# Kernel optimization log

Measured on AMD Instinct MI355X. Metric: run time of the kernel, lower is better.

Reference implementation:

```python
import jax, jax.numpy as jnp
import numpy as np

B, L, N, D, H, R = 4, 4096, 1024, 768, 12, 8
HD = D // H
LORA_SCALE = 16.0 / 8.0
EPS = 1e-5

def _layernorm(x, g, b):
    mu = jnp.mean(x, axis=-1, keepdims=True)
    var = jnp.mean(jnp.square(x - mu), axis=-1, keepdims=True)
    return (x - mu) * jax.lax.rsqrt(var + EPS) * g + b

def setup_inputs() -> dict:
    key = jax.random.key(0)
    ks = jax.random.split(key, 16)
    s = 0.02
    return {
        "text": jax.random.normal(ks[0], (B, L, D), jnp.float32),
        "regions": jax.random.normal(ks[1], (B, N, D), jnp.float32),
        "region_mask": jax.random.randint(ks[2], (B, N), 0, 2) > 0,
        "Wq": jax.random.normal(ks[3], (D, D), jnp.float32) * s,
        "Aq": jax.random.normal(ks[4], (R, D), jnp.float32) * s,
        "Bq": jax.random.normal(ks[5], (D, R), jnp.float32) * s,
        "Wk": jax.random.normal(ks[6], (D, D), jnp.float32) * s,
        "Wv": jax.random.normal(ks[7], (D, D), jnp.float32) * s,
        "Av": jax.random.normal(ks[8], (R, D), jnp.float32) * s,
        "Bv": jax.random.normal(ks[9], (D, R), jnp.float32) * s,
        "Wo": jax.random.normal(ks[10], (D, D), jnp.float32) * s,
        "bo": jnp.zeros((D,), jnp.float32),
        "gq": jnp.ones((D,), jnp.float32),
        "bq_ln": jnp.zeros((D,), jnp.float32),
        "gkv": jnp.ones((D,), jnp.float32),
        "bkv": jnp.zeros((D,), jnp.float32),
    }

def reference(text, regions, region_mask, Wq, Aq, Bq, Wk, Wv, Av, Bv, Wo, bo, gq, bq_ln, gkv, bkv):
    # pre-norms
    tq = _layernorm(text, gq, bq_ln)          # (B,L,D)
    rk = _layernorm(regions, gkv, bkv)        # (B,N,D)
    # LoRA-adapted projections (weights stored as (out,in), torch convention)
    Q = tq @ Wq.T + LORA_SCALE * ((tq @ Aq.T) @ Bq.T)
    K = rk @ Wk.T
    V = regions @ Wv.T + LORA_SCALE * ((regions @ Av.T) @ Bv.T)
    Q = Q.reshape(B, L, H, HD)
    K = K.reshape(B, N, H, HD)
    V = V.reshape(B, N, H, HD)
    scale = HD ** -0.5
    attn = jnp.einsum('blhd,bnhd->bhln', Q, K) * scale   # (B,H,L,N)
    bad = ~region_mask[:, None, None, :]
    attn = jnp.where(bad, -jnp.inf, attn)
    attn = jax.nn.softmax(attn, axis=-1)
    attn = jnp.nan_to_num(attn, nan=0.0)                 # fully-masked rows -> 0
    # dropout: eval mode (identity)
    out = jnp.einsum('bhln,bnhd->blhd', attn, V).reshape(B, L, D)
    return text + out @ Wo.T + bo
```

## Files before the change

### kernel.cpp

```cpp
#include <hip/hip_runtime.h>
#include <cstdint>
#include <cstddef>

#define B_  4
#define L_  4096
#define N_  1024
#define D_  768
#define H_  12
#define HD_ 64

typedef __bf16 bf16x4 __attribute__((ext_vector_type(4)));
typedef __bf16 bf16x8 __attribute__((ext_vector_type(8)));
typedef float  f32x4  __attribute__((ext_vector_type(4)));
typedef unsigned int u32;

static __device__ __forceinline__ f32x4 mfma16(bf16x8 a, bf16x8 b, f32x4 c) {
    return __builtin_amdgcn_mfma_f32_16x16x32_bf16(a, b, c, 0, 0, 0);
}

static __device__ __forceinline__ void async_cp16(const __bf16* g, const __bf16* l) {
    __builtin_amdgcn_global_load_lds(
        (const __attribute__((address_space(1))) u32*)g,
        (__attribute__((address_space(3))) u32*)l, 16, 0, 0);
}

static __device__ __forceinline__ u32 pkbf(float lo, float hi) {
    union { __bf16 b[2]; u32 u; } r;
    r.b[0] = (__bf16)lo; r.b[1] = (__bf16)hi;
    return r.u;
}


static __device__ __forceinline__ void ln_row(const float* __restrict__ xr,
                                              const float* __restrict__ g,
                                              const float* __restrict__ be,
                                              __bf16* __restrict__ yr)
{
    const int tid = threadIdx.x, lane = tid & 63, wid = tid >> 6;
    float4 v = make_float4(0.f, 0.f, 0.f, 0.f);
    if (tid < 192) v = *(const float4*)(xr + tid * 4);
    float s  = v.x + v.y + v.z + v.w;
    float s2 = v.x * v.x + v.y * v.y + v.z * v.z + v.w * v.w;
#pragma unroll
    for (int off = 32; off > 0; off >>= 1) {
        s  += __shfl_down(s, off);
        s2 += __shfl_down(s2, off);
    }
    __shared__ float red[8];
    if (lane == 0) { red[wid] = s; red[4 + wid] = s2; }
    __syncthreads();
    s  = red[0] + red[1] + red[2] + red[3];
    s2 = red[4] + red[5] + red[6] + red[7];
    const float mean = s * (1.f / D_);
    const float var  = s2 * (1.f / D_) - mean * mean;
    const float rstd = rsqrtf(var + 1e-5f);
    if (tid < 192) {
        const float4 gv = *(const float4*)(g + tid * 4);
        const float4 bv = *(const float4*)(be + tid * 4);
        bf16x4 o;
        o[0] = (__bf16)((v.x - mean) * rstd * gv.x + bv.x);
        o[1] = (__bf16)((v.y - mean) * rstd * gv.y + bv.y);
        o[2] = (__bf16)((v.z - mean) * rstd * gv.z + bv.z);
        o[3] = (__bf16)((v.w - mean) * rstd * gv.w + bv.w);
        *(bf16x4*)(yr + tid * 4) = o;
    }
}

static __device__ __forceinline__ void cast4(const float* __restrict__ in,
                                             __bf16* __restrict__ out, int blk)
{
    const int i = (blk * 256 + threadIdx.x) * 4;
    const float4 v = *(const float4*)(in + i);
    bf16x4 o;
    o[0] = (__bf16)v.x; o[1] = (__bf16)v.y; o[2] = (__bf16)v.z; o[3] = (__bf16)v.w;
    *(bf16x4*)(out + i) = o;
}

static __device__ __forceinline__ void weff4(const float* __restrict__ W,
                                             const float* __restrict__ Bm,
                                             const float* __restrict__ Am,
                                             __bf16* __restrict__ out, int blk)
{
    const int idx = (blk * 256 + threadIdx.x) * 4;
    const int o = idx / D_, i = idx - o * D_;
    const float4 w = *(const float4*)(W + idx);
    float sx = 0.f, sy = 0.f, sz = 0.f, sw = 0.f;
#pragma unroll
    for (int r = 0; r < 8; ++r) {
        const float b = Bm[o * 8 + r];
        const float4 a = *(const float4*)(Am + r * D_ + i);
        sx += b * a.x; sy += b * a.y; sz += b * a.z; sw += b * a.w;
    }
    bf16x4 ov;
    ov[0] = (__bf16)(w.x + 2.f * sx);
    ov[1] = (__bf16)(w.y + 2.f * sy);
    ov[2] = (__bf16)(w.z + 2.f * sz);
    ov[3] = (__bf16)(w.w + 2.f * sw);
    *(bf16x4*)(out + idx) = ov;
}

static __device__ __forceinline__ void compact_mask(const int* __restrict__ mask,
                                                    int* __restrict__ idxm,
                                                    int* __restrict__ Nv)
{
    const int tid = threadIdx.x, lane = tid & 63, wid = tid >> 6;
    const int4 mv = *(const int4*)(mask + tid * 4);
    const int v0 = mv.x != 0, v1 = mv.y != 0, v2 = mv.z != 0, v3 = mv.w != 0;
    const int c = v0 + v1 + v2 + v3;
    int incl = c;
#pragma unroll
    for (int off = 1; off < 64; off <<= 1) {
        const int n = __shfl_up(incl, off);
        if (lane >= off) incl += n;
    }
    __shared__ int wsum[4];
    if (lane == 63) wsum[wid] = incl;
    __syncthreads();
    int base = 0;
    for (int w = 0; w < wid; ++w) base += wsum[w];
    int p = base + incl - c;
    idxm[tid * 4 + 0] = v0 ? p : -1; p += v0;
    idxm[tid * 4 + 1] = v1 ? p : -1; p += v1;
    idxm[tid * 4 + 2] = v2 ? p : -1; p += v2;
    idxm[tid * 4 + 3] = v3 ? p : -1; p += v3;
    if (tid == 255) *Nv = p;
}

__global__ __launch_bounds__(256) void prologue_kernel(
    const float* __restrict__ text, const float* __restrict__ regions,
    const int* __restrict__ mask,
    const float* __restrict__ Wq, const float* __restrict__ Aq, const float* __restrict__ Bq,
    const float* __restrict__ Wv, const float* __restrict__ Av, const float* __restrict__ Bv,
    const float* __restrict__ Wk, const float* __restrict__ Wo,
    const float* __restrict__ gq, const float* __restrict__ bq,
    const float* __restrict__ gkv, const float* __restrict__ bkv,
    __bf16* __restrict__ tq, __bf16* __restrict__ rk, __bf16* __restrict__ regb,
    __bf16* __restrict__ Weq, __bf16* __restrict__ Wev,
    __bf16* __restrict__ Wkb, __bf16* __restrict__ Wob,
    int* __restrict__ idx_map, int* __restrict__ NvArr)
{
    int bx = blockIdx.x;
    if (bx < B_ * L_) { ln_row(text + (size_t)bx * D_, gq, bq, tq + (size_t)bx * D_); return; }
    bx -= B_ * L_;
    if (bx < B_ * N_) { ln_row(regions + (size_t)bx * D_, gkv, bkv, rk + (size_t)bx * D_); return; }
    bx -= B_ * N_;
    if (bx < 3072) { cast4(regions, regb, bx); return; }
    bx -= 3072;
    if (bx < 576) { weff4(Wq, Bq, Aq, Weq, bx); return; }
    bx -= 576;
    if (bx < 576) { weff4(Wv, Bv, Av, Wev, bx); return; }
    bx -= 576;
    if (bx < 576) { cast4(Wk, Wkb, bx); return; }
    bx -= 576;
    if (bx < 576) { cast4(Wo, Wob, bx); return; }
    bx -= 576;
    compact_mask(mask + bx * N_, idx_map + bx * N_, NvArr + bx);
}

template <int EPI, typename CT>
static __device__ __forceinline__ void gemm_body(__bf16* sm,
                                                 const __bf16* __restrict__ A,
                                                 const __bf16* __restrict__ W,
                                                 CT* __restrict__ C,
                                                 const float* __restrict__ resid,
                                                 const float* __restrict__ bias,
                                                 const int* __restrict__ idxm,
                                                 int mb0, int nb0)
{
    const int tid = threadIdx.x, wid = tid >> 6, lane = tid & 63;
    const int lr = lane & 15, g = lane >> 4;
    const int wm = wid >> 1, wn = wid & 1;

    auto skey2 = [](int row) { return (row >> 1) & 3; };

    auto stage = [&](int kb, int buf) {
        __bf16* as = sm + buf * 8192;
        __bf16* bs = as + 4096;
#pragma unroll
        for (int j = 0; j < 2; ++j) {
            const int s = wid * 64 + lane + j * 256;
            const int row = s >> 2;
            const int c = (s & 3) ^ skey2(row);
            const int dst = (wid * 64 + j * 256) * 8;
            async_cp16(A + (size_t)(mb0 + row) * D_ + kb * 32 + c * 8, as + dst);
            async_cp16(W + (size_t)(nb0 + row) * D_ + kb * 32 + c * 8, bs + dst);
        }
    };

    f32x4 acc[4][4] = {};

    stage(0, 0);
    asm volatile("s_waitcnt vmcnt(0)" ::: "memory");
    __syncthreads();

    for (int kb = 0; kb < D_ / 32; ++kb) {
        const int buf = kb & 1;
        if (kb < D_ / 32 - 1) stage(kb + 1, buf ^ 1);
        const __bf16* as = sm + buf * 8192;
        const __bf16* bs = as + 4096;
        bf16x8 av[4], wv[4];
#pragma unroll
        for (int mi = 0; mi < 4; ++mi) {
            const int row = wm * 64 + mi * 16 + lr;
            av[mi] = *(const bf16x8*)(as + row * 32 + (g ^ skey2(row)) * 8);
        }
#pragma unroll
        for (int oi = 0; oi < 4; ++oi) {
            const int row = wn * 64 + oi * 16 + lr;
            wv[oi] = *(const bf16x8*)(bs + row * 32 + (g ^ skey2(row)) * 8);
        }
        __builtin_amdgcn_s_setprio(1);
#pragma unroll
        for (int mi = 0; mi < 4; ++mi)
#pragma unroll
            for (int oi = 0; oi < 4; ++oi)
                acc[mi][oi] = mfma16(av[mi], wv[oi], acc[mi][oi]);
        __builtin_amdgcn_s_setprio(0);
        asm volatile("s_waitcnt vmcnt(0)" ::: "memory");
        __syncthreads();
    }

#pragma unroll
    for (int mi = 0; mi < 4; ++mi) {
#pragma unroll
        for (int oi = 0; oi < 4; ++oi) {
#pragma unroll
            for (int r = 0; r < 4; ++r) {
                const int m = mb0 + wm * 64 + mi * 16 + g * 4 + r;
                const int o = nb0 + wn * 64 + oi * 16 + lr;
                float v = acc[mi][oi][r];
                if (EPI == 2)
                    v += resid[(size_t)m * D_ + o] + bias[o];
                if (EPI == 3)
                    v *= 0.125f;
                if (EPI == 4) {
                    const int pos = idxm[m];
                    if (pos >= 0)
                        C[((size_t)((m >> 10) << 10) + pos) * D_ + o] = (CT)v;
                } else if (EPI == 5) {
                    const int pos = idxm[m];
                    if (pos >= 0)
                        C[((size_t)((m >> 10) * H_ + (o >> 6)) * HD_ + (o & 63)) * N_ + pos] = (CT)v;
                } else {
                    C[(size_t)m * D_ + o] = (CT)v;
                }
            }
        }
    }
}

__global__ __launch_bounds__(256) void gemm_qkv(const __bf16* __restrict__ tq,
                                                const __bf16* __restrict__ Weq,
                                                __bf16* __restrict__ Qb,
                                                const __bf16* __restrict__ rk,
                                                const __bf16* __restrict__ Wkb,
                                                __bf16* __restrict__ Kb,
                                                const __bf16* __restrict__ regb,
                                                const __bf16* __restrict__ Wev,
                                                __bf16* __restrict__ Vt,
                                                const int* __restrict__ idx_map)
{
    extern __shared__ __bf16 smem[];
    const int bx = blockIdx.x, ny = blockIdx.y * 128;
    if (bx < 128)      gemm_body<3, __bf16>(smem, tq,   Weq, Qb, nullptr, nullptr, nullptr, bx * 128, ny);
    else if (bx < 160) gemm_body<4, __bf16>(smem, rk,   Wkb, Kb, nullptr, nullptr, idx_map, (bx - 128) * 128, ny);
    else               gemm_body<5, __bf16>(smem, regb, Wev, Vt, nullptr, nullptr, idx_map, (bx - 160) * 128, ny);
}

__global__ __launch_bounds__(256) void gemm_out(const __bf16* __restrict__ A,
                                                const __bf16* __restrict__ W,
                                                float* __restrict__ C,
                                                const float* __restrict__ resid,
                                                const float* __restrict__ bias)
{
    extern __shared__ __bf16 smem[];
    gemm_body<2, float>(smem, A, W, C, resid, bias, nullptr, blockIdx.x * 128, blockIdx.y * 128);
}

__global__ __launch_bounds__(256, 3) void attn_kernel(const __bf16* __restrict__ Qb,
                                                      const __bf16* __restrict__ Kb,
                                                      const __bf16* __restrict__ Vt,
                                                      const int* __restrict__ NvArr,
                                                      __bf16* __restrict__ ctx)
{
    const int bq = blockIdx.x, h = blockIdx.y, b = blockIdx.z;
    const int tid = threadIdx.x, wid = tid >> 6, lane = tid & 63;
    const int lr = lane & 15, g = lane >> 4;

    const int Nv = NvArr[b];
    const int ntiles = (Nv + 63) >> 6;

    __shared__ float maskadd[N_];
    __shared__ __align__(16) __bf16 kbuf[2][4096];
    __shared__ __align__(16) __bf16 vbuf[2][4096];

    for (int i = tid; i < N_; i += 256)
        maskadd[i] = (i < Nv) ? 0.f : -1e30f;

    const int hoff = h * HD_;
    const int bN = b * N_;
    const size_t bhHD = ((size_t)b * H_ + h) * HD_;

    auto skey = [](int row) { return (row & 3) | (((row >> 3) & 1) << 2); };

    auto stage = [&](int t, int bsel) {
        const int n0 = t * 64;
#pragma unroll
        for (int j = 0; j < 2; ++j) {
            const int s = wid * 64 + lane + j * 256;
            const int row = s >> 3;
            const int ks = (s & 7) ^ skey(row);
            const int dst = (wid * 64 + j * 256) * 8;
            async_cp16(Kb + ((size_t)(bN + n0 + row) * D_ + hoff + ks * 8), &kbuf[bsel][dst]);
            async_cp16(Vt + (bhHD + row) * N_ + n0 + ks * 8, &vbuf[bsel][dst]);
        }
    };

    const int q0 = bq * 128 + wid * 32;
    bf16x8 qa[2][2];
#pragma unroll
    for (int qf = 0; qf < 2; ++qf) {
        const __bf16* qptr = Qb + ((size_t)b * L_ + q0 + qf * 16 + lr) * D_ + hoff + g * 8;
        qa[qf][0] = *(const bf16x8*)(qptr);
        qa[qf][1] = *(const bf16x8*)(qptr + 32);
    }

    f32x4 acc[2][4] = {};
    float ssum[2] = {0.f, 0.f};

    if (ntiles > 0) {
        stage(0, 0);
        asm volatile("s_waitcnt vmcnt(0)" ::: "memory");
        __syncthreads();

        for (int t = 0; t < ntiles; ++t) {
            const int buf = t & 1;
            if (t + 1 < ntiles) stage(t + 1, buf ^ 1);

            const __bf16* kb = kbuf[buf];
            const __bf16* vb = vbuf[buf];

            f32x4 mv[4];
#pragma unroll
            for (int kt = 0; kt < 4; ++kt)
                mv[kt] = *(const f32x4*)&maskadd[t * 64 + (kt >> 1) * 32 + g * 8 + (kt & 1) * 4];

            bf16x8 kf[4][2];
#pragma unroll
            for (int kt = 0; kt < 4; ++kt) {
                const int row = (kt >> 1) * 32 + (lr >> 2) * 8 + (kt & 1) * 4 + (lr & 3);
                const int kx = skey(row);
#pragma unroll
                for (int kc = 0; kc < 2; ++kc)
                    kf[kt][kc] = *(const bf16x8*)((const char*)kb + row * 128 + ((((kc * 4) + g) ^ kx) << 4));
            }

            bf16x8 pa[2][2];
#pragma unroll
            for (int qf = 0; qf < 2; ++qf) {
                f32x4 s4[4];
                __builtin_amdgcn_s_setprio(1);
#pragma unroll
                for (int kt = 0; kt < 4; ++kt) {
                    f32x4 z = {};
                    s4[kt] = mfma16(kf[kt][0], qa[qf][0], z);
                    s4[kt] = mfma16(kf[kt][1], qa[qf][1], s4[kt]);
                }
                __builtin_amdgcn_s_setprio(0);

                float p[4][4];
                float tsum = 0.f;
#pragma unroll
                for (int kt = 0; kt < 4; ++kt)
#pragma unroll
                    for (int r = 0; r < 4; ++r) {
                        p[kt][r] = __expf(s4[kt][r] + mv[kt][r]);
                        tsum += p[kt][r];
                    }
                tsum += __shfl_xor(tsum, 16);
                tsum += __shfl_xor(tsum, 32);
                ssum[qf] += tsum;

#pragma unroll
                for (int c = 0; c < 2; ++c) {
                    union { u32 w[4]; bf16x8 v; } pu;
#pragma unroll
                    for (int m = 0; m < 4; ++m) {
                        const int kt = 2 * c + (m >> 1);
                        pu.w[m] = pkbf(p[kt][2 * (m & 1)], p[kt][2 * (m & 1) + 1]);
                    }
                    pa[qf][c] = pu.v;
                }
            }

            __builtin_amdgcn_s_setprio(1);
#pragma unroll
            for (int dt = 0; dt < 4; ++dt) {
                const int d = dt * 16 + lr;
                const int vx = skey(d);
#pragma unroll
                for (int c = 0; c < 2; ++c) {
                    const bf16x8 vf = *(const bf16x8*)((const char*)vb + d * 128 + ((((c * 4) + g) ^ vx) << 4));
                    acc[0][dt] = mfma16(pa[0][c], vf, acc[0][dt]);
                    acc[1][dt] = mfma16(pa[1][c], vf, acc[1][dt]);
                }
            }
            __builtin_amdgcn_s_setprio(0);

            asm volatile("s_waitcnt vmcnt(0)" ::: "memory");
            __syncthreads();
        }
    }

#pragma unroll
    for (int qf = 0; qf < 2; ++qf) {
        const float inv = (ssum[qf] > 0.f) ? 1.f / ssum[qf] : 0.f;
        float iv[4];
#pragma unroll
        for (int r = 0; r < 4; ++r) iv[r] = __shfl(inv, g * 4 + r);
#pragma unroll
        for (int dt = 0; dt < 4; ++dt)
#pragma unroll
            for (int r = 0; r < 4; ++r) {
                const int q = q0 + qf * 16 + g * 4 + r;
                ctx[((size_t)b * L_ + q) * D_ + hoff + dt * 16 + lr] = (__bf16)(acc[qf][dt][r] * iv[r]);
            }
    }
}

extern "C" void kernel_launch(void* const* d_in, const int* in_sizes, int n_in,
                              void* d_out, int out_size, void* d_ws, size_t ws_size,
                              hipStream_t stream)
{
    const float* text    = (const float*)d_in[0];
    const float* regions = (const float*)d_in[1];
    const int*   mask    = (const int*)d_in[2];
    const float* Wq  = (const float*)d_in[3];
    const float* Aq  = (const float*)d_in[4];
    const float* Bq  = (const float*)d_in[5];
    const float* Wk  = (const float*)d_in[6];
    const float* Wv  = (const float*)d_in[7];
    const float* Av  = (const float*)d_in[8];
    const float* Bv  = (const float*)d_in[9];
    const float* Wo  = (const float*)d_in[10];
    const float* bo  = (const float*)d_in[11];
    const float* gq  = (const float*)d_in[12];
    const float* bq  = (const float*)d_in[13];
    const float* gkv = (const float*)d_in[14];
    const float* bkv = (const float*)d_in[15];

    const size_t BLD = (size_t)B_ * L_ * D_;
    const size_t BND = (size_t)B_ * N_ * D_;
    const size_t DD  = (size_t)D_ * D_;
    __bf16* ws   = (__bf16*)d_ws;
    __bf16* tq   = ws;
    __bf16* rk   = tq + BLD;
    __bf16* Qb   = rk + BND;
    __bf16* Kb   = Qb + BLD;
    __bf16* Vt   = Kb + BND;
    __bf16* ctx  = Vt + BND;
    __bf16* regb = ctx + BLD;
    __bf16* Weq  = regb + BND;
    __bf16* Wev  = Weq + DD;
    __bf16* Wkb  = Wev + DD;
    __bf16* Wob  = Wkb + DD;
    int* idx_map = (int*)(Wob + DD);
    int* NvArr   = idx_map + B_ * N_;

    const int smB = 32768;
    const int nProBlocks = B_ * L_ + B_ * N_ + 3072 + 576 * 4 + B_;

    prologue_kernel<<<dim3(nProBlocks), 256, 0, stream>>>(
        text, regions, mask, Wq, Aq, Bq, Wv, Av, Bv, Wk, Wo,
        gq, bq, gkv, bkv, tq, rk, regb, Weq, Wev, Wkb, Wob, idx_map, NvArr);
    gemm_qkv<<<dim3(192, D_ / 128), 256, smB, stream>>>(tq, Weq, Qb, rk, Wkb, Kb, regb, Wev, Vt, idx_map);
    attn_kernel<<<dim3(L_ / 128, H_, B_), 256, 0, stream>>>(Qb, Kb, Vt, NvArr, ctx);
    gemm_out<<<dim3((B_ * L_) / 128, D_ / 128), 256, smB, stream>>>(ctx, Wob, (float*)d_out, text, bo);
}
```

Baseline: 154.3 us.

## Compact masked region rows before K/V projections and fuse region LN with cast

The prologue now writes layer-normed and bf16-cast region rows directly into compacted positions. Each block finds its position by counting the kept mask entries before its row. The K and V GEMM blocks whose row tile lies beyond the valid count exit early, and the separate cast pass and index-map scatter epilogues are removed. This is meant to cut projection work on masked regions and one pass over the region tensor. In exchange, every region block repeats a serial ballot-count over the mask, and rows past the valid count are left unwritten, so the attention kernel must ignore them.

```diff
diff --git a/kernel.cpp b/kernel.cpp
--- a/kernel.cpp
+++ b/kernel.cpp
@@ -66,6 +66,60 @@
     }
 }
 
+static __device__ __forceinline__ void ln_cast_region(const float* __restrict__ xr,
+                                                      const int* __restrict__ maskb, int n,
+                                                      const float* __restrict__ g,
+                                                      const float* __restrict__ be,
+                                                      __bf16* __restrict__ rk_base,
+                                                      __bf16* __restrict__ regb_base)
+{
+    const int tid = threadIdx.x, lane = tid & 63, wid = tid >> 6;
+    const bool keep = maskb[n] != 0;
+
+    __shared__ int cnt[4];
+    int pos = 0;
+    for (int i0 = 0; i0 < n; i0 += 256) {
+        const int i = i0 + tid;
+        const int mv = (i < n) ? maskb[i] : 0;
+        const unsigned long long bal = __ballot(mv != 0);
+        if (lane == 0) cnt[wid] = __popcll(bal);
+        __syncthreads();
+        pos += cnt[0] + cnt[1] + cnt[2] + cnt[3];
+        __syncthreads();
+    }
+    if (!keep) return;
+
+    float4 v = make_float4(0.f, 0.f, 0.f, 0.f);
+    if (tid < 192) v = *(const float4*)(xr + tid * 4);
+    float s  = v.x + v.y + v.z + v.w;
+    float s2 = v.x * v.x + v.y * v.y + v.z * v.z + v.w * v.w;
+#pragma unroll
+    for (int off = 32; off > 0; off >>= 1) {
+        s  += __shfl_down(s, off);
+        s2 += __shfl_down(s2, off);
+    }
+    __shared__ float red[8];
+    if (lane == 0) { red[wid] = s; red[4 + wid] = s2; }
+    __syncthreads();
+    s  = red[0] + red[1] + red[2] + red[3];
+    s2 = red[4] + red[5] + red[6] + red[7];
+    const float mean = s * (1.f / D_);
+    const float var  = s2 * (1.f / D_) - mean * mean;
+    const float rstd = rsqrtf(var + 1e-5f);
+    if (tid < 192) {
+        const float4 gv = *(const float4*)(g + tid * 4);
+        const float4 bv = *(const float4*)(be + tid * 4);
+        bf16x4 o, c;
+        o[0] = (__bf16)((v.x - mean) * rstd * gv.x + bv.x);
+        o[1] = (__bf16)((v.y - mean) * rstd * gv.y + bv.y);
+        o[2] = (__bf16)((v.z - mean) * rstd * gv.z + bv.z);
+        o[3] = (__bf16)((v.w - mean) * rstd * gv.w + bv.w);
+        c[0] = (__bf16)v.x; c[1] = (__bf16)v.y; c[2] = (__bf16)v.z; c[3] = (__bf16)v.w;
+        *(bf16x4*)(rk_base + (size_t)pos * D_ + tid * 4) = o;
+        *(bf16x4*)(regb_base + (size_t)pos * D_ + tid * 4) = c;
+    }
+}
+
 static __device__ __forceinline__ void cast4(const float* __restrict__ in,
                                              __bf16* __restrict__ out, int blk)
 {
@@ -99,31 +153,18 @@
     *(bf16x4*)(out + idx) = ov;
 }
 
-static __device__ __forceinline__ void compact_mask(const int* __restrict__ mask,
-                                                    int* __restrict__ idxm,
-                                                    int* __restrict__ Nv)
+static __device__ __forceinline__ void count_mask(const int* __restrict__ maskb,
+                                                  int* __restrict__ Nv)
 {
     const int tid = threadIdx.x, lane = tid & 63, wid = tid >> 6;
-    const int4 mv = *(const int4*)(mask + tid * 4);
-    const int v0 = mv.x != 0, v1 = mv.y != 0, v2 = mv.z != 0, v3 = mv.w != 0;
-    const int c = v0 + v1 + v2 + v3;
-    int incl = c;
-#pragma unroll
-    for (int off = 1; off < 64; off <<= 1) {
-        const int n = __shfl_up(incl, off);
-        if (lane >= off) incl += n;
-    }
-    __shared__ int wsum[4];
-    if (lane == 63) wsum[wid] = incl;
+    const int4 mv = *(const int4*)(maskb + tid * 4);
+    int c = (mv.x != 0) + (mv.y != 0) + (mv.z != 0) + (mv.w != 0);
+#pragma unroll
+    for (int off = 32; off > 0; off >>= 1) c += __shfl_down(c, off);
+    __shared__ int w4[4];
+    if (lane == 0) w4[wid] = c;
     __syncthreads();
-    int base = 0;
-    for (int w = 0; w < wid; ++w) base += wsum[w];
-    int p = base + incl - c;
-    idxm[tid * 4 + 0] = v0 ? p : -1; p += v0;
-    idxm[tid * 4 + 1] = v1 ? p : -1; p += v1;
-    idxm[tid * 4 + 2] = v2 ? p : -1; p += v2;
-    idxm[tid * 4 + 3] = v3 ? p : -1; p += v3;
-    if (tid == 255) *Nv = p;
+    if (tid == 0) *Nv = w4[0] + w4[1] + w4[2] + w4[3];
 }
 
 __global__ __launch_bounds__(256) void prologue_kernel(
@@ -137,15 +178,18 @@
     __bf16* __restrict__ tq, __bf16* __restrict__ rk, __bf16* __restrict__ regb,
     __bf16* __restrict__ Weq, __bf16* __restrict__ Wev,
     __bf16* __restrict__ Wkb, __bf16* __restrict__ Wob,
-    int* __restrict__ idx_map, int* __restrict__ NvArr)
+    int* __restrict__ NvArr)
 {
     int bx = blockIdx.x;
     if (bx < B_ * L_) { ln_row(text + (size_t)bx * D_, gq, bq, tq + (size_t)bx * D_); return; }
     bx -= B_ * L_;
-    if (bx < B_ * N_) { ln_row(regions + (size_t)bx * D_, gkv, bkv, rk + (size_t)bx * D_); return; }
+    if (bx < B_ * N_) {
+        const int b = bx >> 10, n = bx & (N_ - 1);
+        ln_cast_region(regions + (size_t)bx * D_, mask + b * N_, n, gkv, bkv,
+                       rk + (size_t)b * N_ * D_, regb + (size_t)b * N_ * D_);
+        return;
+    }
     bx -= B_ * N_;
-    if (bx < 3072) { cast4(regions, regb, bx); return; }
-    bx -= 3072;
     if (bx < 576) { weff4(Wq, Bq, Aq, Weq, bx); return; }
     bx -= 576;
     if (bx < 576) { weff4(Wv, Bv, Av, Wev, bx); return; }
@@ -154,7 +198,7 @@
     bx -= 576;
     if (bx < 576) { cast4(Wo, Wob, bx); return; }
     bx -= 576;
-    compact_mask(mask + bx * N_, idx_map + bx * N_, NvArr + bx);
+    count_mask(mask + bx * N_, NvArr + bx);
 }
 
 template <int EPI, typename CT>
@@ -164,7 +208,6 @@
                                                  CT* __restrict__ C,
                                                  const float* __restrict__ resid,
                                                  const float* __restrict__ bias,
-                                                 const int* __restrict__ idxm,
                                                  int mb0, int nb0)
 {
     const int tid = threadIdx.x, wid = tid >> 6, lane = tid & 63;
@@ -233,14 +276,10 @@
                     v += resid[(size_t)m * D_ + o] + bias[o];
                 if (EPI == 3)
                     v *= 0.125f;
-                if (EPI == 4) {
-                    const int pos = idxm[m];
-                    if (pos >= 0)
-                        C[((size_t)((m >> 10) << 10) + pos) * D_ + o] = (CT)v;
-                } else if (EPI == 5) {
-                    const int pos = idxm[m];
-                    if (pos >= 0)
-                        C[((size_t)((m >> 10) * H_ + (o >> 6)) * HD_ + (o & 63)) * N_ + pos] = (CT)v;
+                if (EPI == 1) {
+                    const size_t idx =
+                        ((size_t)((m >> 10) * H_ + (o >> 6)) * HD_ + (o & 63)) * N_ + (m & (N_ - 1));
+                    C[idx] = (CT)v;
                 } else {
                     C[(size_t)m * D_ + o] = (CT)v;
                 }
@@ -258,13 +297,21 @@
                                                 const __bf16* __restrict__ regb,
                                                 const __bf16* __restrict__ Wev,
                                                 __bf16* __restrict__ Vt,
-                                                const int* __restrict__ idx_map)
+                                                const int* __restrict__ NvArr)
 {
     extern __shared__ __bf16 smem[];
     const int bx = blockIdx.x, ny = blockIdx.y * 128;
-    if (bx < 128)      gemm_body<3, __bf16>(smem, tq,   Weq, Qb, nullptr, nullptr, nullptr, bx * 128, ny);
-    else if (bx < 160) gemm_body<4, __bf16>(smem, rk,   Wkb, Kb, nullptr, nullptr, idx_map, (bx - 128) * 128, ny);
-    else               gemm_body<5, __bf16>(smem, regb, Wev, Vt, nullptr, nullptr, idx_map, (bx - 160) * 128, ny);
+    if (bx < 128) {
+        gemm_body<3, __bf16>(smem, tq, Weq, Qb, nullptr, nullptr, bx * 128, ny);
+    } else if (bx < 160) {
+        const int m0 = (bx - 128) * 128;
+        if ((m0 & (N_ - 1)) >= NvArr[m0 >> 10]) return;
+        gemm_body<0, __bf16>(smem, rk, Wkb, Kb, nullptr, nullptr, m0, ny);
+    } else {
+        const int m0 = (bx - 160) * 128;
+        if ((m0 & (N_ - 1)) >= NvArr[m0 >> 10]) return;
+        gemm_body<1, __bf16>(smem, regb, Wev, Vt, nullptr, nullptr, m0, ny);
+    }
 }
 
 __global__ __launch_bounds__(256) void gemm_out(const __bf16* __restrict__ A,
@@ -274,7 +321,7 @@
                                                 const float* __restrict__ bias)
 {
     extern __shared__ __bf16 smem[];
-    gemm_body<2, float>(smem, A, W, C, resid, bias, nullptr, blockIdx.x * 128, blockIdx.y * 128);
+    gemm_body<2, float>(smem, A, W, C, resid, bias, blockIdx.x * 128, blockIdx.y * 128);
 }
 
 __global__ __launch_bounds__(256, 3) void attn_kernel(const __bf16* __restrict__ Qb,
@@ -464,16 +511,15 @@
     __bf16* Wev  = Weq + DD;
     __bf16* Wkb  = Wev + DD;
     __bf16* Wob  = Wkb + DD;
-    int* idx_map = (int*)(Wob + DD);
-    int* NvArr   = idx_map + B_ * N_;
+    int* NvArr   = (int*)(Wob + DD);
 
     const int smB = 32768;
-    const int nProBlocks = B_ * L_ + B_ * N_ + 3072 + 576 * 4 + B_;
+    const int nProBlocks = B_ * L_ + B_ * N_ + 576 * 4 + B_;
 
     prologue_kernel<<<dim3(nProBlocks), 256, 0, stream>>>(
         text, regions, mask, Wq, Aq, Bq, Wv, Av, Bv, Wk, Wo,
-        gq, bq, gkv, bkv, tq, rk, regb, Weq, Wev, Wkb, Wob, idx_map, NvArr);
-    gemm_qkv<<<dim3(192, D_ / 128), 256, smB, stream>>>(tq, Weq, Qb, rk, Wkb, Kb, regb, Wev, Vt, idx_map);
+        gq, bq, gkv, bkv, tq, rk, regb, Weq, Wev, Wkb, Wob, NvArr);
+    gemm_qkv<<<dim3(192, D_ / 128), 256, smB, stream>>>(tq, Weq, Qb, rk, Wkb, Kb, regb, Wev, Vt, NvArr);
     attn_kernel<<<dim3(L_ / 128, H_, B_), 256, 0, stream>>>(Qb, Kb, Vt, NvArr, ctx);
     gemm_out<<<dim3((B_ * L_) / 128, D_ / 128), 256, smB, stream>>>(ctx, Wob, (float*)d_out, text, bo);
 }
```

Result: faster. 145.7 us (-5.5%).
